# Performance work log

Measured on AMD Instinct MI355X. Metric: run time of the kernel, lower is better.

## Reference

```python
import jax, jax.numpy as jnp
import numpy as np

RADIUS = 0.2
OC = 128   # output_channel
EC = 64    # extra_input_channel


def _select(radius, xyz):
    # xyz: [BT, N, 3] -> idx [BT, N, 8] (nearest point in each octant within radius, else self)
    BT, N, _ = xyz.shape
    jd = radius * radius
    diff = xyz[:, None, :, :] - xyz[:, :, None, :]          # diff[b, n, j] = xyz[b, j] - xyz[b, n]
    dist = jnp.sum(diff * diff, -1)                          # [BT, N, N]
    # torch .int() truncates toward zero; jnp float->int32 cast does the same
    octant = jnp.sum((diff + 1.0).astype(jnp.int32) *
                     jnp.array([4, 2, 1], jnp.int32), -1)    # [BT, N, N]
    eye = jnp.arange(N)
    # self entry gets judge_dist (fallback winner), everything else 1e10
    base = jnp.where(eye[:, None] == eye[None, :],
                     jnp.float32(jd), jnp.float32(1e10))[None]  # [1, N, N]
    valid = (dist > 1e-10) & (dist < jd)
    idx8 = [jnp.argmin(jnp.where((octant == i) & valid, dist, base), -1)
            for i in range(8)]
    return jnp.stack(idx8, -1)                               # [BT, N, 8]


def _gather(p, idx):
    # p: [BT, N, C], idx: [BT, N, 8] -> [BT, N, 8, C]
    return jax.vmap(lambda a, i: a[i])(p, idx)


def _conv12(x, w, b):
    # Conv2d kernel [1,2] stride [1,2]: x [B, C, N, W] -> [B, O, N, W//2]
    B_, C, N, Wd = x.shape
    xp = x.reshape(B_, C, N, Wd // 2, 2)
    return jnp.einsum('bcnpk,ock->bonp', xp, w) + b[None, :, None, None]


def _forward(xyz4, points4, w1a, b1a, w1b, b1b, w1c, b1c, w2a, b2a, w2b, b2b, w2c, b2c):
    B, T, N, _ = xyz4.shape
    xyz = xyz4.reshape(B * T, N, 3)
    pts = points4.reshape(B * T, N, -1)
    idx = _select(RADIUS, xyz)
    g_xyz = _gather(xyz, idx) - xyz[:, :, None, :]           # [BT, N, 8, 3]
    g_pts = jnp.concatenate([g_xyz, _gather(pts, idx)], -1)  # [BT, N, 8, 3+EC]
    x = g_pts.transpose(0, 3, 1, 2)                          # [BT, C, N, 8]
    x = _conv12(x, w1a, b1a)
    x = _conv12(x, w1b, b1b)
    x = _conv12(x, w1c, b1c)                                 # [BT, OC, N, 1]
    new = x[..., 0].transpose(0, 2, 1)                       # [BT, N, OC]
    g_pts2 = jnp.concatenate([g_xyz, _gather(new, idx)], -1) # [BT, N, 8, 3+OC]
    x = g_pts2.transpose(0, 3, 1, 2)
    x = _conv12(x, w2a, b2a)
    x = _conv12(x, w2b, b2b)
    x = _conv12(x, w2c, b2c)                                 # [BT, OC, N, 1]
    new = x[..., 0]                                          # [BT, OC, N]
    out = jnp.concatenate([new, pts.transpose(0, 2, 1)], 1)  # merge='concat'
    out = jax.nn.relu(out).transpose(0, 2, 1).reshape(B, T, N, -1)
    return xyz4, out


def setup_inputs() -> dict:
    key = jax.random.key(0)
    ks = jax.random.split(key, 16)
    B, T, N = 4, 4, 1024
    xyz = jax.random.uniform(ks[0], (B, T, N, 3), jnp.float32)
    points = jax.random.normal(ks[1], (B, T, N, EC), jnp.float32)
    w = lambda k, o, c: jax.random.normal(k, (o, c, 2), jnp.float32) * 0.05
    b = lambda k, o: jax.random.normal(k, (o,), jnp.float32) * 0.05
    return {
        'xyz': xyz, 'points': points,
        'w1a': w(ks[2], OC, 3 + EC), 'b1a': b(ks[3], OC),
        'w1b': w(ks[4], OC, OC),     'b1b': b(ks[5], OC),
        'w1c': w(ks[6], OC, OC),     'b1c': b(ks[7], OC),
        'w2a': w(ks[8], OC, 3 + OC), 'b2a': b(ks[9], OC),
        'w2b': w(ks[10], OC, OC),    'b2b': b(ks[11], OC),
        'w2c': w(ks[12], OC, OC),    'b2c': b(ks[13], OC),
    }


def reference(xyz, points, w1a, b1a, w1b, b1b, w1c, b1c, w2a, b2a, w2b, b2b, w2c, b2c):
    return _forward(xyz, points, w1a, b1a, w1b, b1b, w1c, b1c,
                    w2a, b2a, w2b, b2b, w2c, b2c)
```

## Files before the change

### kernel.cpp

```cpp
#include <hip/hip_runtime.h>
#include <stdint.h>

typedef unsigned int u32;
typedef unsigned long long u64;
typedef unsigned short us;
using short8 = __attribute__((ext_vector_type(8))) short;
using us8    = __attribute__((ext_vector_type(8))) us;
using f32x4  = __attribute__((ext_vector_type(4))) float;

#define BT 16
#define NPT 1024

__device__ __forceinline__ us f2bf(float f) {
    u32 u = __float_as_uint(f);
    u += 0x7fffu + ((u >> 16) & 1u);
    return (us)(u >> 16);
}
__device__ __forceinline__ float bf2f(us v) { return __uint_as_float(((u32)v) << 16); }
__device__ __forceinline__ u32 packbf(float lo, float hi) {
    return (u32)f2bf(lo) | ((u32)f2bf(hi) << 16);
}

__device__ void wprep_a(int tid, const float* __restrict__ w, us* __restrict__ dst,
                        int Cfeat, int Creal, int NOCT) {
    int lane = tid & 63, ct = (tid >> 6) & 7, kt = tid >> 9;
    int o = ct * 16 + (lane & 15);
    int h = lane >> 4;
    int ci = kt * 4 + h;
    int p = (ci >= NOCT) ? 1 : 0;
    int q = ci - p * NOCT;
    us8 v;
#pragma unroll
    for (int j = 0; j < 8; ++j) {
        int c = q * 8 + j;
        int ref = (c < Cfeat) ? c + 3 : ((c < Cfeat + 3) ? c - Cfeat : -1);
        v[j] = (ref >= 0) ? f2bf(w[((size_t)o * Creal + ref) * 2 + p]) : (us)0;
    }
    *(us8*)(dst + (size_t)tid * 8) = v;
}

__device__ void wprep_b(int tid, const float* __restrict__ w, us* __restrict__ dst) {
    int lane = tid & 63, ct = (tid >> 6) & 7, kt = tid >> 9;
    int o = ct * 16 + (lane & 15);
    int k0 = kt * 32 + ((lane >> 4) << 3);
    us8 v;
#pragma unroll
    for (int j = 0; j < 8; ++j) v[j] = f2bf(w[(size_t)o * 256 + k0 + j]);
    *(us8*)(dst + (size_t)tid * 8) = v;
}

__global__ __launch_bounds__(256) void k_prep(
    const float* __restrict__ xyz, const float* __restrict__ pts,
    const float* __restrict__ w1a, us* __restrict__ f1a,
    const float* __restrict__ w1b, us* __restrict__ f1b,
    const float* __restrict__ w1c, us* __restrict__ f1c,
    const float* __restrict__ w2a, us* __restrict__ f2a,
    const float* __restrict__ w2b, us* __restrict__ f2b,
    const float* __restrict__ w2c, us* __restrict__ f2c,
    us* __restrict__ ptsbf, us* __restrict__ newbf, float* __restrict__ outp) {
    const int u2 = blockIdx.x, t = threadIdx.x;
    if (u2 < 92) {
        if (u2 < 10)      wprep_a(u2 * 256 + t, w1a, f1a, 64, 67, 10);
        else if (u2 < 26) wprep_b((u2 - 10) * 256 + t, w1b, f1b);
        else if (u2 < 42) wprep_b((u2 - 26) * 256 + t, w1c, f1c);
        else if (u2 < 60) wprep_a((u2 - 42) * 256 + t, w2a, f2a, 128, 131, 18);
        else if (u2 < 76) wprep_b((u2 - 60) * 256 + t, w2b, f2b);
        else              wprep_b((u2 - 76) * 256 + t, w2c, f2c);
    } else if (u2 < 140) {
        int id = (u2 - 92) * 256 + t;
        ((float4*)outp)[id] = ((const float4*)xyz)[id];
    } else if (u2 < 204) {
        int r = (u2 - 140) * 256 + t;
        const float4* pr = (const float4*)(pts + ((size_t)r << 6));
        u32* dst = (u32*)(ptsbf + (size_t)r * 80);
#pragma unroll
        for (int i = 0; i < 16; ++i) {
            float4 f = pr[i];
            dst[2 * i]     = packbf(f.x, f.y);
            dst[2 * i + 1] = packbf(f.z, f.w);
        }
        const float* xr = xyz + (size_t)r * 3;
        dst[32] = packbf(xr[0], xr[1]);
        dst[33] = packbf(xr[2], 0.f);
#pragma unroll
        for (int i = 34; i < 40; ++i) dst[i] = 0u;
    } else {
        int r = (u2 - 204) * 256 + t;
        u32* dst = (u32*)(newbf + (size_t)r * 144);
        const float* xr = xyz + (size_t)r * 3;
        dst[64] = packbf(xr[0], xr[1]);
        dst[65] = packbf(xr[2], 0.f);
#pragma unroll
        for (int i = 66; i < 72; ++i) dst[i] = 0u;
    }
}

__global__ __launch_bounds__(256) void k_s1(
    const float* __restrict__ xyz, const us* __restrict__ ptsbf,
    u64* __restrict__ keys,
    const us* __restrict__ wfa, const float* __restrict__ ba,
    const us* __restrict__ wfb, const float* __restrict__ bb,
    const us* __restrict__ wfc, const float* __restrict__ bc,
    us* __restrict__ newbf_out) {
    constexpr int KTA = 5, NOCT = 10, RSTR = 80, FIXC = 64, FIXQ = 8;
    __shared__ __align__(16) char smem[24576];
    __shared__ u64 kfin[16][8];
    float* jx  = (float*)smem;
    us* lists  = (us*)(smem + 12288);
    us* abuf   = (us*)smem;
    us* cbuf   = (us*)(smem + 16384);

    const int u = (int)(((blockIdx.x & 7u) << 7) | (blockIdx.x >> 3));
    const int t = threadIdx.x, wid = t >> 6, lane = t & 63;
    const int li = lane & 15, h = lane >> 4;
    const int g0 = u * 16;
    const int b = u >> 6;
    const int nb0 = g0 & (NPT - 1);
    const float* xg = xyz + (size_t)b * 3072;
    const us* fb = ptsbf + (size_t)b * NPT * RSTR;

    for (int i = t; i < 768; i += 256) ((float4*)jx)[i] = ((const float4*)xg)[i];
    if (t < 128)
        kfin[t >> 3][t & 7] = ((u64)__float_as_uint(0.04f) << 32) | (u32)(nb0 + (t >> 3));
    __syncthreads();

    us* wl = lists + wid * 1024;
    for (int nn = 0; nn < 4; ++nn) {
        const int n_loc = wid * 4 + nn;
        const int nb = nb0 + n_loc;
        const float xn = jx[nb * 3], yn = jx[nb * 3 + 1], zn = jx[nb * 3 + 2];
        u32 cnt = 0;
        for (int i = 0; i < 16; ++i) {
            int j = i * 64 + lane;
            float dx = __fadd_rn(jx[j * 3 + 0], -xn);
            float dy = __fadd_rn(jx[j * 3 + 1], -yn);
            float dz = __fadd_rn(jx[j * 3 + 2], -zn);
            float d = __fadd_rn(__fadd_rn(__fmul_rn(dx, dx), __fmul_rn(dy, dy)),
                                __fmul_rn(dz, dz));
            bool valid = (d > 1e-10f) && (d < 0.04f);
            u64 m = __ballot(valid);
            if (valid) {
                u32 off = __builtin_amdgcn_mbcnt_lo((u32)m, 0);
                off = __builtin_amdgcn_mbcnt_hi((u32)(m >> 32), off);
                wl[cnt + off] = (us)j;
            }
            cnt += (u32)__popcll(m);
        }
        for (u32 idx = lane; idx < cnt; idx += 64) {
            int j = wl[idx];
            float dx = __fadd_rn(jx[j * 3 + 0], -xn);
            float dy = __fadd_rn(jx[j * 3 + 1], -yn);
            float dz = __fadd_rn(jx[j * 3 + 2], -zn);
            float d = __fadd_rn(__fadd_rn(__fmul_rn(dx, dx), __fmul_rn(dy, dy)),
                                __fmul_rn(dz, dz));
            int oct = ((int)__fadd_rn(dx, 1.0f)) * 4 + ((int)__fadd_rn(dy, 1.0f)) * 2 +
                      ((int)__fadd_rn(dz, 1.0f));
            u64 key = ((u64)__float_as_uint(d) << 32) | (u32)j;
            atomicMin(&kfin[n_loc][oct], key);
        }
    }
    __syncthreads();

    if (t < 128)
        keys[(((size_t)g0 + (t >> 3)) << 3) + (t & 7)] = kfin[t >> 3][t & 7];
    const int n_loc_c = wid * 4 + (li >> 2), pos = li & 3;
    const int J0 = (int)(u32)kfin[n_loc_c][2 * pos];
    const int J1 = (int)(u32)kfin[n_loc_c][2 * pos + 1];
    const int N = nb0 + n_loc_c;
    __syncthreads();

    const us* row0 = fb + (size_t)J0 * RSTR;
    const us* row1 = fb + (size_t)J1 * RSTR;
    us8 xn8 = *(const us8*)(fb + (size_t)N * RSTR + FIXC);
    const float xn0 = bf2f(xn8[0]), xn1 = bf2f(xn8[1]), xn2 = bf2f(xn8[2]);

    f32x4 acc[8];
#pragma unroll
    for (int ct = 0; ct < 8; ++ct) {
        float bv = ba[ct * 16 + li];
        acc[ct] = f32x4{bv, bv, bv, bv};
    }
    for (int kt = 0; kt < KTA; ++kt) {
        int ci = kt * 4 + h;
        int q = (ci >= NOCT) ? ci - NOCT : ci;
        const us* rp = (ci >= NOCT) ? row1 : row0;
        us8 v = *(const us8*)(rp + q * 8);
        if (q == FIXQ) {
            v[0] = f2bf(__fadd_rn(bf2f(v[0]), -xn0));
            v[1] = f2bf(__fadd_rn(bf2f(v[1]), -xn1));
            v[2] = f2bf(__fadd_rn(bf2f(v[2]), -xn2));
        }
        short8 a = __builtin_bit_cast(short8, v);
        const us* wk = wfa + (size_t)kt * 4096;
#pragma unroll
        for (int ct = 0; ct < 8; ++ct) {
            short8 w = *(const short8*)(wk + ((size_t)ct * 64 + lane) * 8);
            acc[ct] = __builtin_amdgcn_mfma_f32_16x16x32_bf16(a, w, acc[ct], 0, 0, 0);
        }
    }
    {
        u32* dst = (u32*)abuf;
        int mbase = wid * 16 + (h << 2);
        int mr0 = mbase >> 1, mr1 = mr0 + 1;
#pragma unroll
        for (int ct = 0; ct < 8; ++ct) {
            f32x4 av = acc[ct];
            u32 p0 = packbf(av[0], av[1]);
            u32 p1 = packbf(av[2], av[3]);
            dst[((mr0 >> 4) * 8 + ct) * 256 + ((mr0 & 15) + ((li >> 2) << 4)) * 4 + (li & 3)] = p0;
            dst[((mr1 >> 4) * 8 + ct) * 256 + ((mr1 & 15) + ((li >> 2) << 4)) * 4 + (li & 3)] = p1;
        }
    }
    __syncthreads();

    const int mtB = wid >> 1, ctbB = (wid & 1) * 4;
    f32x4 accB[4];
#pragma unroll
    for (int cc = 0; cc < 4; ++cc) {
        float bv = bb[(ctbB + cc) * 16 + li];
        accB[cc] = f32x4{bv, bv, bv, bv};
    }
    for (int kt = 0; kt < 8; ++kt) {
        short8 a = *(const short8*)(abuf + (((size_t)mtB * 8 + kt) * 64 + lane) * 8);
        const us* wk = wfb + ((size_t)kt * 8 + ctbB) * 512;
#pragma unroll
        for (int cc = 0; cc < 4; ++cc) {
            short8 w = *(const short8*)(wk + ((size_t)cc * 64 + lane) * 8);
            accB[cc] = __builtin_amdgcn_mfma_f32_16x16x32_bf16(a, w, accB[cc], 0, 0, 0);
        }
    }
    {
        u32* dst = (u32*)cbuf;
        int mbase = mtB * 16 + (h << 2);
        int mr0 = mbase >> 1, mr1 = mr0 + 1;
#pragma unroll
        for (int cc = 0; cc < 4; ++cc) {
            int ct = ctbB + cc;
            f32x4 av = accB[cc];
            u32 p0 = packbf(av[0], av[1]);
            u32 p1 = packbf(av[2], av[3]);
            dst[ct * 256 + (mr0 + ((li >> 2) << 4)) * 4 + (li & 3)] = p0;
            dst[ct * 256 + (mr1 + ((li >> 2) << 4)) * 4 + (li & 3)] = p1;
        }
    }
    __syncthreads();

    f32x4 accC[2];
#pragma unroll
    for (int cc = 0; cc < 2; ++cc) {
        float bv = bc[(wid * 2 + cc) * 16 + li];
        accC[cc] = f32x4{bv, bv, bv, bv};
    }
    for (int kt = 0; kt < 8; ++kt) {
        short8 a = *(const short8*)(cbuf + ((size_t)kt * 64 + lane) * 8);
        const us* wk = wfc + ((size_t)kt * 8 + wid * 2) * 512;
#pragma unroll
        for (int cc = 0; cc < 2; ++cc) {
            short8 w = *(const short8*)(wk + ((size_t)cc * 64 + lane) * 8);
            accC[cc] = __builtin_amdgcn_mfma_f32_16x16x32_bf16(a, w, accC[cc], 0, 0, 0);
        }
    }
#pragma unroll
    for (int cc = 0; cc < 2; ++cc) {
        int o = (wid * 2 + cc) * 16 + li;
#pragma unroll
        for (int r = 0; r < 4; ++r) {
            int gg = g0 + h * 4 + r;
            newbf_out[(size_t)gg * 144 + o] = f2bf(accC[cc][r]);
        }
    }
}

__global__ __launch_bounds__(256) void k_s2(
    const float* __restrict__ pts, const us* __restrict__ feat,
    const u32* __restrict__ keys32,
    const us* __restrict__ wfa, const float* __restrict__ ba,
    const us* __restrict__ wfb, const float* __restrict__ bb,
    const us* __restrict__ wfc, const float* __restrict__ bc,
    float* __restrict__ outp) {
    constexpr int KTA = 9, NOCT = 18, RSTR = 144, FIXC = 128, FIXQ = 16;
    __shared__ us abuf[2 * 8 * 512];
    __shared__ us cbuf[1 * 8 * 512];

    const int u = (int)(((blockIdx.x & 7u) << 7) | (blockIdx.x >> 3));
    const int t = threadIdx.x, wid = t >> 6, lane = t & 63;
    const int li = lane & 15, h = lane >> 4;
    const int m0 = u * 64;
    const int g0 = u * 16;
    const int b = u >> 6;
    const us* fb = feat + (size_t)b * NPT * RSTR;

    const int m = m0 + wid * 16 + li;
    const int g = m >> 2, pos = m & 3;
    const int J0 = (int)keys32[((size_t)g * 8 + 2 * pos) * 2];
    const int J1 = (int)keys32[((size_t)g * 8 + 2 * pos + 1) * 2];
    const int N = g & (NPT - 1);

    const us* row0 = fb + (size_t)J0 * RSTR;
    const us* row1 = fb + (size_t)J1 * RSTR;
    us8 xn8 = *(const us8*)(fb + (size_t)N * RSTR + FIXC);
    const float xn0 = bf2f(xn8[0]), xn1 = bf2f(xn8[1]), xn2 = bf2f(xn8[2]);

    f32x4 acc[8];
#pragma unroll
    for (int ct = 0; ct < 8; ++ct) {
        float bv = ba[ct * 16 + li];
        acc[ct] = f32x4{bv, bv, bv, bv};
    }
    for (int kt = 0; kt < KTA; ++kt) {
        int ci = kt * 4 + h;
        int q = (ci >= NOCT) ? ci - NOCT : ci;
        const us* rp = (ci >= NOCT) ? row1 : row0;
        us8 v = *(const us8*)(rp + q * 8);
        if (q == FIXQ) {
            v[0] = f2bf(__fadd_rn(bf2f(v[0]), -xn0));
            v[1] = f2bf(__fadd_rn(bf2f(v[1]), -xn1));
            v[2] = f2bf(__fadd_rn(bf2f(v[2]), -xn2));
        }
        short8 a = __builtin_bit_cast(short8, v);
        const us* wk = wfa + (size_t)kt * 4096;
#pragma unroll
        for (int ct = 0; ct < 8; ++ct) {
            short8 w = *(const short8*)(wk + ((size_t)ct * 64 + lane) * 8);
            acc[ct] = __builtin_amdgcn_mfma_f32_16x16x32_bf16(a, w, acc[ct], 0, 0, 0);
        }
    }
    {
        u32* dst = (u32*)abuf;
        int mbase = wid * 16 + (h << 2);
        int mr0 = mbase >> 1, mr1 = mr0 + 1;
#pragma unroll
        for (int ct = 0; ct < 8; ++ct) {
            f32x4 av = acc[ct];
            u32 p0 = packbf(av[0], av[1]);
            u32 p1 = packbf(av[2], av[3]);
            dst[((mr0 >> 4) * 8 + ct) * 256 + ((mr0 & 15) + ((li >> 2) << 4)) * 4 + (li & 3)] = p0;
            dst[((mr1 >> 4) * 8 + ct) * 256 + ((mr1 & 15) + ((li >> 2) << 4)) * 4 + (li & 3)] = p1;
        }
    }
    __syncthreads();

    const int mtB = wid >> 1, ctbB = (wid & 1) * 4;
    f32x4 accB[4];
#pragma unroll
    for (int cc = 0; cc < 4; ++cc) {
        float bv = bb[(ctbB + cc) * 16 + li];
        accB[cc] = f32x4{bv, bv, bv, bv};
    }
    for (int kt = 0; kt < 8; ++kt) {
        short8 a = *(const short8*)(abuf + (((size_t)mtB * 8 + kt) * 64 + lane) * 8);
        const us* wk = wfb + ((size_t)kt * 8 + ctbB) * 512;
#pragma unroll
        for (int cc = 0; cc < 4; ++cc) {
            short8 w = *(const short8*)(wk + ((size_t)cc * 64 + lane) * 8);
            accB[cc] = __builtin_amdgcn_mfma_f32_16x16x32_bf16(a, w, accB[cc], 0, 0, 0);
        }
    }
    {
        u32* dst = (u32*)cbuf;
        int mbase = mtB * 16 + (h << 2);
        int mr0 = mbase >> 1, mr1 = mr0 + 1;
#pragma unroll
        for (int cc = 0; cc < 4; ++cc) {
            int ct = ctbB + cc;
            f32x4 av = accB[cc];
            u32 p0 = packbf(av[0], av[1]);
            u32 p1 = packbf(av[2], av[3]);
            dst[ct * 256 + (mr0 + ((li >> 2) << 4)) * 4 + (li & 3)] = p0;
            dst[ct * 256 + (mr1 + ((li >> 2) << 4)) * 4 + (li & 3)] = p1;
        }
    }
    __syncthreads();

    f32x4 accC[2];
#pragma unroll
    for (int cc = 0; cc < 2; ++cc) {
        float bv = bc[(wid * 2 + cc) * 16 + li];
        accC[cc] = f32x4{bv, bv, bv, bv};
    }
    for (int kt = 0; kt < 8; ++kt) {
        short8 a = *(const short8*)(cbuf + ((size_t)kt * 64 + lane) * 8);
        const us* wk = wfc + ((size_t)kt * 8 + wid * 2) * 512;
#pragma unroll
        for (int cc = 0; cc < 2; ++cc) {
            short8 w = *(const short8*)(wk + ((size_t)cc * 64 + lane) * 8);
            accC[cc] = __builtin_amdgcn_mfma_f32_16x16x32_bf16(a, w, accC[cc], 0, 0, 0);
        }
    }
#pragma unroll
    for (int cc = 0; cc < 2; ++cc) {
        int o = (wid * 2 + cc) * 16 + li;
#pragma unroll
        for (int r = 0; r < 4; ++r) {
            int gg = g0 + h * 4 + r;
            outp[(size_t)49152 + (size_t)gg * 192 + o] = fmaxf(accC[cc][r], 0.f);
        }
    }

    {
        int r = t >> 4, q = t & 15;
        float4 v = ((const float4*)(pts + ((size_t)(g0 + r) << 6)))[q];
        v.x = fmaxf(v.x, 0.0f);
        v.y = fmaxf(v.y, 0.0f);
        v.z = fmaxf(v.z, 0.0f);
        v.w = fmaxf(v.w, 0.0f);
        *(float4*)(outp + 49152 + (size_t)(g0 + r) * 192 + 128 + q * 4) = v;
    }
}

extern "C" void kernel_launch(void* const* d_in, const int* in_sizes, int n_in,
                              void* d_out, int out_size, void* d_ws, size_t ws_size,
                              hipStream_t stream) {
    const float* xyz = (const float*)d_in[0];
    const float* pts = (const float*)d_in[1];
    const float* w1a = (const float*)d_in[2];
    const float* b1a = (const float*)d_in[3];
    const float* w1b = (const float*)d_in[4];
    const float* b1b = (const float*)d_in[5];
    const float* w1c = (const float*)d_in[6];
    const float* b1c = (const float*)d_in[7];
    const float* w2a = (const float*)d_in[8];
    const float* b2a = (const float*)d_in[9];
    const float* w2b = (const float*)d_in[10];
    const float* b2b = (const float*)d_in[11];
    const float* w2c = (const float*)d_in[12];
    const float* b2c = (const float*)d_in[13];
    float* outp = (float*)d_out;

    char* ws = (char*)d_ws;
    u64* keys = (u64*)ws;
    const u32* keys32 = (const u32*)ws;
    us* wf1a = (us*)(ws + 1048576);
    us* wf1b = (us*)(ws + 1089536);
    us* wf1c = (us*)(ws + 1155072);
    us* wf2a = (us*)(ws + 1220608);
    us* wf2b = (us*)(ws + 1294336);
    us* wf2c = (us*)(ws + 1359872);
    us* ptsbf = (us*)(ws + 2097152);
    us* newbf = (us*)(ws + 5242880);

    k_prep<<<268, 256, 0, stream>>>(xyz, pts, w1a, wf1a, w1b, wf1b, w1c, wf1c,
                                    w2a, wf2a, w2b, wf2b, w2c, wf2c,
                                    ptsbf, newbf, outp);
    k_s1<<<1024, 256, 0, stream>>>(xyz, ptsbf, keys,
                                   wf1a, b1a, wf1b, b1b, wf1c, b1c, newbf);
    k_s2<<<1024, 256, 0, stream>>>(pts, newbf, keys32,
                                   wf2a, b2a, wf2b, b2b, wf2c, b2c, outp);
}
```

Before: 61.36 us.

## Hold candidate points in registers and fuse neighbor search into direct atomics

Each thread now loads four candidate points straight from global memory into registers, and the 16 query points are staged in a small shared array. The old scheme copied the whole point cloud into shared memory and ran a two-pass compaction per wave. Every thread now tests its four candidates against all 16 queries and issues atomicMin directly on valid hits. This removes the shared-memory xyz staging, the ballot/list compaction and the second distance pass. The cost is more divergent branches and possibly more contended shared atomics across waves.

```diff
diff --git a/kernel.cpp b/kernel.cpp
--- a/kernel.cpp
+++ b/kernel.cpp
@@ -105,10 +105,9 @@
     constexpr int KTA = 5, NOCT = 10, RSTR = 80, FIXC = 64, FIXQ = 8;
     __shared__ __align__(16) char smem[24576];
     __shared__ u64 kfin[16][8];
-    float* jx  = (float*)smem;
-    us* lists  = (us*)(smem + 12288);
-    us* abuf   = (us*)smem;
-    us* cbuf   = (us*)(smem + 16384);
+    __shared__ float snn[48];
+    us* abuf = (us*)smem;
+    us* cbuf = (us*)(smem + 16384);
 
     const int u = (int)(((blockIdx.x & 7u) << 7) | (blockIdx.x >> 3));
     const int t = threadIdx.x, wid = t >> 6, lane = t & 63;
@@ -119,44 +118,34 @@
     const float* xg = xyz + (size_t)b * 3072;
     const us* fb = ptsbf + (size_t)b * NPT * RSTR;
 
-    for (int i = t; i < 768; i += 256) ((float4*)jx)[i] = ((const float4*)xg)[i];
+    const int j0 = (wid << 8) + (lane << 2);
+    float4 c0 = *(const float4*)(xg + (size_t)j0 * 3);
+    float4 c1 = *(const float4*)(xg + (size_t)j0 * 3 + 4);
+    float4 c2 = *(const float4*)(xg + (size_t)j0 * 3 + 8);
+    const float jxc[4] = {c0.x, c0.w, c1.z, c2.y};
+    const float jyc[4] = {c0.y, c1.x, c1.w, c2.z};
+    const float jzc[4] = {c0.z, c1.y, c2.x, c2.w};
+
+    if (t < 48) snn[t] = xg[(size_t)nb0 * 3 + t];
     if (t < 128)
         kfin[t >> 3][t & 7] = ((u64)__float_as_uint(0.04f) << 32) | (u32)(nb0 + (t >> 3));
     __syncthreads();
 
-    us* wl = lists + wid * 1024;
-    for (int nn = 0; nn < 4; ++nn) {
-        const int n_loc = wid * 4 + nn;
-        const int nb = nb0 + n_loc;
-        const float xn = jx[nb * 3], yn = jx[nb * 3 + 1], zn = jx[nb * 3 + 2];
-        u32 cnt = 0;
-        for (int i = 0; i < 16; ++i) {
-            int j = i * 64 + lane;
-            float dx = __fadd_rn(jx[j * 3 + 0], -xn);
-            float dy = __fadd_rn(jx[j * 3 + 1], -yn);
-            float dz = __fadd_rn(jx[j * 3 + 2], -zn);
+    for (int i = 0; i < 16; ++i) {
+        const float xn = snn[i * 3], yn = snn[i * 3 + 1], zn = snn[i * 3 + 2];
+#pragma unroll
+        for (int jj = 0; jj < 4; ++jj) {
+            float dx = __fadd_rn(jxc[jj], -xn);
+            float dy = __fadd_rn(jyc[jj], -yn);
+            float dz = __fadd_rn(jzc[jj], -zn);
             float d = __fadd_rn(__fadd_rn(__fmul_rn(dx, dx), __fmul_rn(dy, dy)),
                                 __fmul_rn(dz, dz));
-            bool valid = (d > 1e-10f) && (d < 0.04f);
-            u64 m = __ballot(valid);
-            if (valid) {
-                u32 off = __builtin_amdgcn_mbcnt_lo((u32)m, 0);
-                off = __builtin_amdgcn_mbcnt_hi((u32)(m >> 32), off);
-                wl[cnt + off] = (us)j;
+            if (d > 1e-10f && d < 0.04f) {
+                int oct = ((int)__fadd_rn(dx, 1.0f)) * 4 + ((int)__fadd_rn(dy, 1.0f)) * 2 +
+                          ((int)__fadd_rn(dz, 1.0f));
+                u64 key = ((u64)__float_as_uint(d) << 32) | (u32)(j0 + jj);
+                atomicMin(&kfin[i][oct], key);
             }
-            cnt += (u32)__popcll(m);
-        }
-        for (u32 idx = lane; idx < cnt; idx += 64) {
-            int j = wl[idx];
-            float dx = __fadd_rn(jx[j * 3 + 0], -xn);
-            float dy = __fadd_rn(jx[j * 3 + 1], -yn);
-            float dz = __fadd_rn(jx[j * 3 + 2], -zn);
-            float d = __fadd_rn(__fadd_rn(__fmul_rn(dx, dx), __fmul_rn(dy, dy)),
-                                __fmul_rn(dz, dz));
-            int oct = ((int)__fadd_rn(dx, 1.0f)) * 4 + ((int)__fadd_rn(dy, 1.0f)) * 2 +
-                      ((int)__fadd_rn(dz, 1.0f));
-            u64 key = ((u64)__float_as_uint(d) << 32) | (u32)j;
-            atomicMin(&kfin[n_loc][oct], key);
         }
     }
     __syncthreads();
```

Result: faster. 53.11 us (median of 2 runs) (-13.4%).
